# Kernel optimization log

Measured on AMD Instinct MI355X. Metric: run time of the kernel, lower is better.

## Reference

```python
import jax, jax.numpy as jnp
import numpy as np

NC = 80
CONF = 0.25
IOU_T = 0.45
MAX_DET = 100
ATTN_RES = 14
NUM_BASE = 5
TOPK = 1024          # candidate pre-filter (EfficientNMS-style)
SCALE = 0.25         # spatial_scale of ROIAlign


def setup_inputs() -> dict:
    key = jax.random.key(0)
    k1, k2, k3, k4 = jax.random.split(key, 4)
    B, A = 4, 25200
    test = jax.random.uniform(k1, (B, A, 5 + NC), dtype=jnp.float32)
    # scale boxes to image coords: cx,cy in [0,608), w,h in [0,120)
    box_scale = jnp.concatenate([jnp.array([608., 608., 120., 120.], jnp.float32),
                                 jnp.ones(1 + NC, jnp.float32)])
    test = test * box_scale
    attn = jax.random.normal(k2, (B, A, NUM_BASE * ATTN_RES * ATTN_RES), dtype=jnp.float32)
    bases = jax.random.normal(k3, (B, NUM_BASE - 1, 160, 160), dtype=jnp.float32)
    sem = jax.random.normal(k4, (B, 1, 160, 160), dtype=jnp.float32)
    return {"test": test, "attn": attn, "bases": bases, "sem": sem}


def _iou_matrix(b):
    # b: [K,4] xyxy
    area = jnp.clip(b[:, 2] - b[:, 0], 0) * jnp.clip(b[:, 3] - b[:, 1], 0)
    lt = jnp.maximum(b[:, None, :2], b[None, :, :2])
    rb = jnp.minimum(b[:, None, 2:], b[None, :, 2:])
    wh = jnp.clip(rb - lt, 0)
    inter = wh[..., 0] * wh[..., 1]
    return inter / (area[:, None] + area[None, :] - inter + 1e-9)


def _nms_single(boxes, scores):
    # boxes [A,4], scores [A,NC]. Class-aware greedy NMS over top-K candidates.
    flat = scores.reshape(-1)
    flat = jnp.where(flat > CONF, flat, -jnp.inf)
    top_s, top_i = jax.lax.top_k(flat, TOPK)
    anchor = top_i // NC
    cls = top_i % NC
    cb = boxes[anchor]                                   # [K,4]
    sup = (_iou_matrix(cb) > IOU_T) & (cls[:, None] == cls[None, :])

    def step(valid, _):
        s = jnp.where(valid, top_s, -jnp.inf)
        j = jnp.argmax(s)
        ok = jnp.isfinite(s[j])
        nv = (valid & ~sup[j]).at[j].set(False)
        return jnp.where(ok, nv, valid), (j, ok)

    _, (sel, selok) = jax.lax.scan(step, jnp.isfinite(top_s), None, length=MAX_DET)
    dboxes = jnp.where(selok[:, None], cb[sel], 0.)
    dscores = jnp.where(selok, top_s[sel], 0.)
    dcls = jnp.where(selok, cls[sel], 0).astype(jnp.int32)
    didx = jnp.where(selok, anchor[sel], 0).astype(jnp.int32)
    return selok.sum().astype(jnp.int32), dboxes, dscores, dcls, didx


def _roi_align(feat, rois, bidx, oh, ow, scale):
    # feat [B,C,H,W], rois [N,4] xyxy (input coords), half_pixel transform,
    # avg mode, 1 sample/bin (adaptive ratio = 1 here since bins < 1 px).
    N = rois.shape[0]
    B, C, H, W = feat.shape
    x1 = rois[:, 0] * scale - 0.5
    y1 = rois[:, 1] * scale - 0.5
    x2 = rois[:, 2] * scale - 0.5
    y2 = rois[:, 3] * scale - 0.5
    ys = y1[:, None] + (jnp.arange(oh, dtype=feat.dtype) + 0.5) * ((y2 - y1) / oh)[:, None]
    xs = x1[:, None] + (jnp.arange(ow, dtype=feat.dtype) + 0.5) * ((x2 - x1) / ow)[:, None]

    def axis(coord, dim):
        valid = (coord > -1.0) & (coord < dim)
        c = jnp.clip(coord, 0.0, dim - 1.0)
        lo = jnp.floor(c)
        hi = jnp.clip(lo + 1, 0, dim - 1)
        return lo.astype(jnp.int32), hi.astype(jnp.int32), c - lo, valid

    y0, y1i, wy, vy = axis(ys, H)
    x0, x1i, wx, vx = axis(xs, W)
    featn = feat[bidx]                                   # [N,C,H,W]
    n = jnp.arange(N)[:, None, None]

    def g(Y, X):  # -> [N,oh,ow,C]
        return featn[n, :, Y[:, :, None], X[:, None, :]]

    wy_ = wy[:, :, None, None]
    wx_ = wx[:, None, :, None]
    val = (g(y0, x0) * (1 - wy_) * (1 - wx_) + g(y0, x1i) * (1 - wy_) * wx_
           + g(y1i, x0) * wy_ * (1 - wx_) + g(y1i, x1i) * wy_ * wx_)
    val = jnp.where((vy[:, :, None] & vx[:, None, :])[..., None], val, 0.)
    return jnp.transpose(val, (0, 3, 1, 2))                # [N,C,oh,ow]


def _forward(test, attn, bases_in, sem):
    bases = jnp.concatenate([bases_in, sem], axis=1)       # [B,5,H,W]
    conv = jnp.array([[1, 0, 1, 0], [0, 1, 0, 1],
                      [-0.5, 0, 0.5, 0], [0, -0.5, 0, 0.5]], test.dtype)
    boxes = test[:, :, :4] @ conv                          # cxcywh -> xyxy
    scores = test[:, :, 5:5 + NC] * test[:, :, 4:5]
    _, dboxes, dscores, dcls, didx = jax.vmap(_nms_single)(boxes, scores)
    B, P, H, W = bases.shape
    bidx = jnp.repeat(jnp.arange(B), MAX_DET)              # [B*D]
    box_i = didx.reshape(-1)
    sel_boxes = boxes[bidx, box_i]                         # [N,4]
    sel_masks = attn[bidx, box_i]                          # [N,980]
    pooled = _roi_align(bases, sel_boxes, bidx, H, W, SCALE)  # [N,5,H,W]
    coeffs = sel_masks.reshape(-1, NUM_BASE, ATTN_RES, ATTN_RES)
    coeffs = jax.image.resize(coeffs, (coeffs.shape[0], NUM_BASE, H, W), 'linear')
    coeffs = jax.nn.softmax(coeffs, axis=1)
    masks = jax.nn.sigmoid((pooled * coeffs).sum(axis=1).reshape(B, MAX_DET, H * W))
    return jnp.concatenate([dboxes, dscores[..., None],
                            dcls.astype(test.dtype)[..., None], masks], axis=-1)


def reference(test, attn, bases, sem):
    return _forward(test, attn, bases, sem)
```

## Files before the change

kernel.cpp:

```cpp
#include <hip/hip_runtime.h>
#include <stdint.h>

#define B_   4
#define A_   25200
#define NC_  80
#define ROW_ 85
#define ATT_ 980
#define MAXDET_ 100
#define TOPK_ 1024
#define CAP_  4096
#define OUTSTRIDE_ 25606
#define HW_ 160
#define HWHW_ 25600
#define CONF_ 0.25f
#define IOUT_ 0.45f

#define WS_HIST 0
#define WS_CNT  4096
#define WS_TB   4160
#define WS_NTOP 4224
#define WS_CAND 8192
#define WS_TOPV 139264
#define WS_TOPA 155648
#define WS_TOPC 172032
#define WS_CB   188416
#define WS_SUP  253952
#define WS_DETA 778240

typedef unsigned long long u64;
typedef unsigned u32;

__global__ void k_clear(char* w) {
    int i = blockIdx.x * 256 + threadIdx.x;
    if (i < 1028) ((u32*)w)[i] = 0u;
}

__global__ void k_hist(const float* __restrict__ test, char* __restrict__ w) {
    int b = blockIdx.y;
    __shared__ u32 h[256];
    if (threadIdx.x < 256) h[threadIdx.x] = 0u;
    __syncthreads();
    const int total = A_ * NC_;
    for (int e = blockIdx.x * 256 + threadIdx.x; e < total; e += 128 * 256) {
        u32 a = (u32)e / 80u;
        u32 c = (u32)e - a * 80u;
        const float* row = test + ((size_t)b * A_ + a) * ROW_;
        float s = row[5 + c] * row[4];
        if (s > CONF_) {
            u32 key = __float_as_uint(s);
            int wb = (int)(key >> 17) - 7936;
            wb = wb < 0 ? 0 : (wb > 255 ? 255 : wb);
            atomicAdd(&h[wb], 1u);
        }
    }
    __syncthreads();
    u32* hist = (u32*)(w + WS_HIST);
    if (threadIdx.x < 256 && h[threadIdx.x]) atomicAdd(&hist[b * 256 + threadIdx.x], h[threadIdx.x]);
}

__global__ void k_thresh(char* w) {
    if (threadIdx.x < B_) {
        int b = threadIdx.x;
        const u32* h = (const u32*)(w + WS_HIST) + b * 256;
        u32 cum = 0; int wtb = 0;
        for (int i = 255; i >= 0; --i) {
            cum += h[i];
            if (cum >= TOPK_) { wtb = i; break; }
        }
        ((int*)(w + WS_TB))[b] = wtb;
    }
}

__global__ void k_collect(const float* __restrict__ test, char* __restrict__ w) {
    int b = blockIdx.y;
    int wtb = ((const int*)(w + WS_TB))[b];
    u32* cnt = (u32*)(w + WS_CNT);
    u64* cand = (u64*)(w + WS_CAND);
    const int total = A_ * NC_;
    for (int e = blockIdx.x * 256 + threadIdx.x; e < total; e += 128 * 256) {
        u32 a = (u32)e / 80u;
        u32 c = (u32)e - a * 80u;
        const float* row = test + ((size_t)b * A_ + a) * ROW_;
        float s = row[5 + c] * row[4];
        if (s > CONF_) {
            u32 key = __float_as_uint(s);
            int wb = (int)(key >> 17) - 7936;
            wb = wb < 0 ? 0 : (wb > 255 ? 255 : wb);
            if (wb >= wtb) {
                u32 pos = atomicAdd(&cnt[b], 1u);
                if (pos < CAP_)
                    cand[(size_t)b * CAP_ + pos] = ((u64)key << 32) | (u64)(0xFFFFFFFFu - (u32)e);
            }
        }
    }
}

__global__ __launch_bounds__(1024) void k_sort(const float* __restrict__ test, char* __restrict__ w) {
    int b = blockIdx.x;
    __shared__ u64 sm[CAP_];
    u32 cnt = ((const u32*)(w + WS_CNT))[b];
    int n = cnt < CAP_ ? (int)cnt : CAP_;
    const u64* cand = (const u64*)(w + WS_CAND) + (size_t)b * CAP_;
    for (int i = threadIdx.x; i < CAP_; i += 1024) sm[i] = (i < n) ? cand[i] : 0ull;
    __syncthreads();
    for (int k = 2; k <= CAP_; k <<= 1) {
        for (int j = k >> 1; j > 0; j >>= 1) {
            for (int t = threadIdx.x; t < CAP_; t += 1024) {
                int ixj = t ^ j;
                if (ixj > t) {
                    u64 a = sm[t], c = sm[ixj];
                    bool desc = ((t & k) == 0);
                    if (desc ? (a < c) : (a > c)) { sm[t] = c; sm[ixj] = a; }
                }
            }
            __syncthreads();
        }
    }
    int ntop = n < TOPK_ ? n : TOPK_;
    if (threadIdx.x == 0) ((int*)(w + WS_NTOP))[b] = ntop;
    if (threadIdx.x < TOPK_) {
        int i = threadIdx.x;
        float* topv = (float*)(w + WS_TOPV);
        int* topa = (int*)(w + WS_TOPA);
        int* topc = (int*)(w + WS_TOPC);
        float4* cb = (float4*)(w + WS_CB);
        if (i < ntop) {
            u64 v = sm[i];
            u32 key = (u32)(v >> 32);
            u32 idx = 0xFFFFFFFFu - (u32)(v & 0xFFFFFFFFull);
            u32 anchor = idx / 80u;
            u32 cls = idx - anchor * 80u;
            const float* tr = test + ((size_t)b * A_ + anchor) * ROW_;
            float cx = tr[0], cy = tr[1], ww = tr[2], hh = tr[3];
            float4 box;
            box.x = cx - 0.5f * ww; box.y = cy - 0.5f * hh;
            box.z = cx + 0.5f * ww; box.w = cy + 0.5f * hh;
            topv[b * TOPK_ + i] = __uint_as_float(key);
            topa[b * TOPK_ + i] = (int)anchor;
            topc[b * TOPK_ + i] = (int)cls;
            cb[b * TOPK_ + i] = box;
        } else {
            topv[b * TOPK_ + i] = 0.f;
            topa[b * TOPK_ + i] = 0;
            topc[b * TOPK_ + i] = 0;
            cb[b * TOPK_ + i] = make_float4(0.f, 0.f, 0.f, 0.f);
        }
    }
}

__device__ __forceinline__ bool sup_pair(float4 a, float4 b, int ca, int cbb) {
#pragma clang fp contract(off)
    if (ca != cbb) return false;
    float areaA = fmaxf(a.z - a.x, 0.f) * fmaxf(a.w - a.y, 0.f);
    float areaB = fmaxf(b.z - b.x, 0.f) * fmaxf(b.w - b.y, 0.f);
    float ltx = fmaxf(a.x, b.x), lty = fmaxf(a.y, b.y);
    float rbx = fminf(a.z, b.z), rby = fminf(a.w, b.w);
    float iw = fmaxf(rbx - ltx, 0.f), ih = fmaxf(rby - lty, 0.f);
    float inter = iw * ih;
    float iou = inter / (((areaA + areaB) - inter) + 1e-9f);
    return iou > IOUT_;
}

__global__ void k_sup(char* __restrict__ w) {
    int b = blockIdx.y;
    int t = blockIdx.x * 256 + threadIdx.x;
    int row = t >> 4, chunk = t & 15;
    const float4* cb = (const float4*)(w + WS_CB) + (size_t)b * TOPK_;
    const int* topc = (const int*)(w + WS_TOPC) + (size_t)b * TOPK_;
    float4 rb = cb[row];
    int rc = topc[row];
    u64 bits = 0ull;
    int base = chunk * 64;
    for (int cc = 0; cc < 64; ++cc) {
        if (sup_pair(rb, cb[base + cc], rc, topc[base + cc])) bits |= (1ull << cc);
    }
    ((u64*)(w + WS_SUP))[((size_t)b * TOPK_ + row) * 16 + chunk] = bits;
}

__global__ void k_nms(char* __restrict__ w, float* __restrict__ out) {
    int b = blockIdx.x;
    int lane = threadIdx.x;
    int ntop = ((const int*)(w + WS_NTOP))[b];
    const u64* sup = (const u64*)(w + WS_SUP);
    __shared__ int selA[MAXDET_];
    __shared__ int okA[MAXDET_];
    u32 valid = 0u;
    for (int t = 0; t < 16; ++t)
        if (lane * 16 + t < ntop) valid |= (1u << t);
    for (int k = 0; k < MAXDET_; ++k) {
        u64 bal = __ballot(valid != 0u);
        if (bal == 0ull) {
            if (lane == 0) { selA[k] = 0; okA[k] = 0; }
            continue;
        }
        int L = __ffsll(bal) - 1;
        u32 vL = (u32)__shfl((int)valid, L);
        int j = L * 16 + (__ffs(vL & 0xFFFFu) - 1);
        u64 chunk = sup[((size_t)b * TOPK_ + j) * 16 + (lane >> 2)];
        u32 s16 = (u32)(chunk >> ((lane & 3) * 16)) & 0xFFFFu;
        valid &= ~s16;
        if (lane == L) valid &= ~(1u << (j & 15));
        if (lane == 0) { selA[k] = j; okA[k] = 1; }
    }
    __syncthreads();
    const float* topv = (const float*)(w + WS_TOPV) + (size_t)b * TOPK_;
    const int* topa = (const int*)(w + WS_TOPA) + (size_t)b * TOPK_;
    const int* topc = (const int*)(w + WS_TOPC) + (size_t)b * TOPK_;
    const float4* cb = (const float4*)(w + WS_CB) + (size_t)b * TOPK_;
    int* deta = (int*)(w + WS_DETA);
    for (int k = lane; k < MAXDET_; k += 64) {
        int ok = okA[k], s = selA[k];
        float b0 = 0, b1 = 0, b2 = 0, b3 = 0, sc = 0; int cls_ = 0, anc = 0;
        if (ok) {
            float4 bb = cb[s];
            b0 = bb.x; b1 = bb.y; b2 = bb.z; b3 = bb.w;
            sc = topv[s]; cls_ = topc[s]; anc = topa[s];
        }
        size_t o = ((size_t)(b * MAXDET_ + k)) * OUTSTRIDE_;
        out[o + 0] = b0; out[o + 1] = b1; out[o + 2] = b2; out[o + 3] = b3;
        out[o + 4] = sc; out[o + 5] = (float)cls_;
        deta[b * MAXDET_ + k] = anc;
    }
}

__global__ void k_mask(const float* __restrict__ test, const float* __restrict__ attn,
                       const float* __restrict__ bases, const float* __restrict__ sem,
                       const char* __restrict__ w, float* __restrict__ out) {
    int roi = blockIdx.x;
    int b = roi / MAXDET_;
    int anchor = ((const int*)(w + WS_DETA))[roi];
    const float* t = test + ((size_t)b * A_ + anchor) * ROW_;
    float cx = t[0], cy = t[1], ww = t[2], hh = t[3];
    float bx1 = cx - 0.5f * ww, by1 = cy - 0.5f * hh;
    float bx2 = cx + 0.5f * ww, by2 = cy + 0.5f * hh;
    float rx1 = bx1 * 0.25f - 0.5f, ry1 = by1 * 0.25f - 0.5f;
    float rx2 = bx2 * 0.25f - 0.5f, ry2 = by2 * 0.25f - 0.5f;
    float xstep = (rx2 - rx1) / 160.f, ystep = (ry2 - ry1) / 160.f;

    __shared__ float att[5 * 196];
    __shared__ float sxw[HW_], syw[HW_], rzw[HW_];
    __shared__ int sxlo[HW_], sxhi[HW_], sylo[HW_], syhi[HW_];
    __shared__ int sxv[HW_], syv[HW_], rzlo[HW_];

    const float* arow = attn + ((size_t)b * A_ + anchor) * ATT_;
    for (int i = threadIdx.x; i < ATT_; i += 256) att[i] = arow[i];
    if (threadIdx.x < HW_) {
        int i = threadIdx.x;
        float coord = rx1 + (i + 0.5f) * xstep;
        sxv[i] = (coord > -1.0f) && (coord < 160.0f);
        float c = fminf(fmaxf(coord, 0.f), 159.f);
        float lo = floorf(c);
        sxlo[i] = (int)lo; sxhi[i] = min((int)lo + 1, 159); sxw[i] = c - lo;
        coord = ry1 + (i + 0.5f) * ystep;
        syv[i] = (coord > -1.0f) && (coord < 160.0f);
        c = fminf(fmaxf(coord, 0.f), 159.f);
        lo = floorf(c);
        sylo[i] = (int)lo; syhi[i] = min((int)lo + 1, 159); syw[i] = c - lo;
        float f = (i + 0.5f) * (14.f / 160.f) - 0.5f;
        float rc = fminf(fmaxf(f, 0.f), 13.f);
        float rlo = floorf(rc);
        rzlo[i] = (int)rlo; rzw[i] = rc - rlo;
    }
    __syncthreads();

    const float* bp[5];
    bp[0] = bases + ((size_t)b * 4 + 0) * HWHW_;
    bp[1] = bases + ((size_t)b * 4 + 1) * HWHW_;
    bp[2] = bases + ((size_t)b * 4 + 2) * HWHW_;
    bp[3] = bases + ((size_t)b * 4 + 3) * HWHW_;
    bp[4] = sem + (size_t)b * HWHW_;

    size_t obase = (size_t)roi * OUTSTRIDE_ + 6;
    int pstart = blockIdx.y * (HWHW_ / 8);
    int pend = pstart + (HWHW_ / 8);
    for (int p = pstart + (int)threadIdx.x; p < pend; p += 256) {
        int y = p / HW_, x = p - y * HW_;
        int ylo = sylo[y], yhi = syhi[y]; float wy = syw[y];
        int xlo = sxlo[x], xhi = sxhi[x]; float wx = sxw[x];
        bool v = sxv[x] && syv[y];
        float w00 = (1.f - wy) * (1.f - wx), w01 = (1.f - wy) * wx;
        float w10 = wy * (1.f - wx), w11 = wy * wx;
        int i00 = ylo * HW_ + xlo, i01 = ylo * HW_ + xhi;
        int i10 = yhi * HW_ + xlo, i11 = yhi * HW_ + xhi;
        float pooled[5];
#pragma unroll
        for (int c5 = 0; c5 < 5; ++c5) {
            float g = bp[c5][i00] * w00 + bp[c5][i01] * w01 + bp[c5][i10] * w10 + bp[c5][i11] * w11;
            pooled[c5] = v ? g : 0.f;
        }
        int cylo = rzlo[y]; float cwy = rzw[y]; int cyhi = min(cylo + 1, 13);
        int cxlo = rzlo[x]; float cwx = rzw[x]; int cxhi = min(cxlo + 1, 13);
        float c00 = (1.f - cwy) * (1.f - cwx), c01 = (1.f - cwy) * cwx;
        float c10 = cwy * (1.f - cwx), c11 = cwy * cwx;
        int j00 = cylo * 14 + cxlo, j01 = cylo * 14 + cxhi;
        int j10 = cyhi * 14 + cxlo, j11 = cyhi * 14 + cxhi;
        float cf[5]; float m = -1e30f;
#pragma unroll
        for (int c5 = 0; c5 < 5; ++c5) {
            const float* ap = att + c5 * 196;
            float g = ap[j00] * c00 + ap[j01] * c01 + ap[j10] * c10 + ap[j11] * c11;
            cf[c5] = g; m = fmaxf(m, g);
        }
        float se = 0.f, dot = 0.f;
#pragma unroll
        for (int c5 = 0; c5 < 5; ++c5) {
            float e = __expf(cf[c5] - m);
            se += e; dot += pooled[c5] * e;
        }
        dot /= se;
        out[obase + p] = 1.f / (1.f + __expf(-dot));
    }
}

extern "C" void kernel_launch(void* const* d_in, const int* in_sizes, int n_in,
                              void* d_out, int out_size, void* d_ws, size_t ws_size,
                              hipStream_t stream) {
    const float* test = (const float*)d_in[0];
    const float* attn = (const float*)d_in[1];
    const float* bases = (const float*)d_in[2];
    const float* sem = (const float*)d_in[3];
    float* out = (float*)d_out;
    char* w = (char*)d_ws;

    k_clear<<<5, 256, 0, stream>>>(w);
    k_hist<<<dim3(128, B_), 256, 0, stream>>>(test, w);
    k_thresh<<<1, 64, 0, stream>>>(w);
    k_collect<<<dim3(128, B_), 256, 0, stream>>>(test, w);
    k_sort<<<B_, 1024, 0, stream>>>(test, w);
    k_sup<<<dim3(64, B_), 256, 0, stream>>>(w);
    k_nms<<<B_, 64, 0, stream>>>(w, out);
    k_mask<<<dim3(B_ * MAXDET_, 8), 256, 0, stream>>>(test, attn, bases, sem, w, out);
}
```

Measured before the change: 709.4 us.

## Fuse sort, suppression and NMS into one block kernel; fold threshold into collect

Removes the threshold kernel by computing a suffix-sum over the histogram inside each collect block. Merges sort, suppression-matrix build and greedy NMS into one 1024-thread kernel per batch that keeps candidates in shared memory and evaluates IoU on the fly for only the chosen row at each step. The bitonic sort now runs on the next power of two at or above the candidate count instead of a fixed 4096. This cuts three launches and the global suppression matrix, but adds two block-wide barriers per NMS step and a serial scan by thread 0.

Measured after the change: 694.9 us. 1.02x faster.

```diff
diff --git a/kernel.cpp b/kernel.cpp
--- a/kernel.cpp
+++ b/kernel.cpp
@@ -17,15 +17,8 @@
 
 #define WS_HIST 0
 #define WS_CNT  4096
-#define WS_TB   4160
-#define WS_NTOP 4224
 #define WS_CAND 8192
-#define WS_TOPV 139264
-#define WS_TOPA 155648
-#define WS_TOPC 172032
-#define WS_CB   188416
-#define WS_SUP  253952
-#define WS_DETA 778240
+#define WS_DETA 139264
 
 typedef unsigned long long u64;
 typedef unsigned u32;
@@ -58,22 +51,32 @@
     if (threadIdx.x < 256 && h[threadIdx.x]) atomicAdd(&hist[b * 256 + threadIdx.x], h[threadIdx.x]);
 }
 
-__global__ void k_thresh(char* w) {
-    if (threadIdx.x < B_) {
-        int b = threadIdx.x;
-        const u32* h = (const u32*)(w + WS_HIST) + b * 256;
-        u32 cum = 0; int wtb = 0;
-        for (int i = 255; i >= 0; --i) {
-            cum += h[i];
-            if (cum >= TOPK_) { wtb = i; break; }
-        }
-        ((int*)(w + WS_TB))[b] = wtb;
-    }
-}
-
 __global__ void k_collect(const float* __restrict__ test, char* __restrict__ w) {
     int b = blockIdx.y;
-    int wtb = ((const int*)(w + WS_TB))[b];
+    __shared__ u32 s[256];
+    __shared__ int swtb;
+    const u32* hist = (const u32*)(w + WS_HIST) + (size_t)b * 256;
+    if (threadIdx.x < 256) s[threadIdx.x] = hist[threadIdx.x];
+    if (threadIdx.x == 0) swtb = 0;
+    __syncthreads();
+    for (int off = 1; off < 256; off <<= 1) {
+        u32 v = 0;
+        if (threadIdx.x < 256) {
+            v = s[threadIdx.x];
+            if (threadIdx.x + off < 256) v += s[threadIdx.x + off];
+        }
+        __syncthreads();
+        if (threadIdx.x < 256) s[threadIdx.x] = v;
+        __syncthreads();
+    }
+    if (threadIdx.x < 256) {
+        u32 Si = s[threadIdx.x];
+        u32 Sn = (threadIdx.x == 255) ? 0u : s[threadIdx.x + 1];
+        if (Si >= TOPK_ && Sn < TOPK_) swtb = threadIdx.x;
+    }
+    __syncthreads();
+    int wtb = swtb;
+
     u32* cnt = (u32*)(w + WS_CNT);
     u64* cand = (u64*)(w + WS_CAND);
     const int total = A_ * NC_;
@@ -81,9 +84,9 @@
         u32 a = (u32)e / 80u;
         u32 c = (u32)e - a * 80u;
         const float* row = test + ((size_t)b * A_ + a) * ROW_;
-        float s = row[5 + c] * row[4];
-        if (s > CONF_) {
-            u32 key = __float_as_uint(s);
+        float sc = row[5 + c] * row[4];
+        if (sc > CONF_) {
+            u32 key = __float_as_uint(sc);
             int wb = (int)(key >> 17) - 7936;
             wb = wb < 0 ? 0 : (wb > 255 ? 255 : wb);
             if (wb >= wtb) {
@@ -95,17 +98,44 @@
     }
 }
 
-__global__ __launch_bounds__(1024) void k_sort(const float* __restrict__ test, char* __restrict__ w) {
+__device__ __forceinline__ bool sup_pair(float4 a, float4 b, int ca, int cbb) {
+#pragma clang fp contract(off)
+    if (ca != cbb) return false;
+    float areaA = fmaxf(a.z - a.x, 0.f) * fmaxf(a.w - a.y, 0.f);
+    float areaB = fmaxf(b.z - b.x, 0.f) * fmaxf(b.w - b.y, 0.f);
+    float ltx = fmaxf(a.x, b.x), lty = fmaxf(a.y, b.y);
+    float rbx = fminf(a.z, b.z), rby = fminf(a.w, b.w);
+    float iw = fmaxf(rbx - ltx, 0.f), ih = fmaxf(rby - lty, 0.f);
+    float inter = iw * ih;
+    float iou = inter / (((areaA + areaB) - inter) + 1e-9f);
+    return iou > IOUT_;
+}
+
+__global__ __launch_bounds__(1024) void k_sortnms(const float* __restrict__ test,
+                                                  char* __restrict__ w,
+                                                  float* __restrict__ out) {
     int b = blockIdx.x;
+    int tid = threadIdx.x;
     __shared__ u64 sm[CAP_];
+    __shared__ float4 cbs[TOPK_];
+    __shared__ float tvs[TOPK_];
+    __shared__ int tcs[TOPK_];
+    __shared__ int tas[TOPK_];
+    __shared__ u64 wmask[16];
+    __shared__ int selA[MAXDET_];
+    __shared__ u32 okA[MAXDET_];
+    __shared__ int sj;
+
     u32 cnt = ((const u32*)(w + WS_CNT))[b];
     int n = cnt < CAP_ ? (int)cnt : CAP_;
+    int n2 = 1024;
+    while (n2 < n) n2 <<= 1;
     const u64* cand = (const u64*)(w + WS_CAND) + (size_t)b * CAP_;
-    for (int i = threadIdx.x; i < CAP_; i += 1024) sm[i] = (i < n) ? cand[i] : 0ull;
-    __syncthreads();
-    for (int k = 2; k <= CAP_; k <<= 1) {
+    for (int i = tid; i < n2; i += 1024) sm[i] = (i < n) ? cand[i] : 0ull;
+    __syncthreads();
+    for (int k = 2; k <= n2; k <<= 1) {
         for (int j = k >> 1; j > 0; j >>= 1) {
-            for (int t = threadIdx.x; t < CAP_; t += 1024) {
+            for (int t = tid; t < n2; t += 1024) {
                 int ixj = t ^ j;
                 if (ixj > t) {
                     u64 a = sm[t], c = sm[ixj];
@@ -117,13 +147,8 @@
         }
     }
     int ntop = n < TOPK_ ? n : TOPK_;
-    if (threadIdx.x == 0) ((int*)(w + WS_NTOP))[b] = ntop;
-    if (threadIdx.x < TOPK_) {
-        int i = threadIdx.x;
-        float* topv = (float*)(w + WS_TOPV);
-        int* topa = (int*)(w + WS_TOPA);
-        int* topc = (int*)(w + WS_TOPC);
-        float4* cb = (float4*)(w + WS_CB);
+    {
+        int i = tid;
         if (i < ntop) {
             u64 v = sm[i];
             u32 key = (u32)(v >> 32);
@@ -135,86 +160,48 @@
             float4 box;
             box.x = cx - 0.5f * ww; box.y = cy - 0.5f * hh;
             box.z = cx + 0.5f * ww; box.w = cy + 0.5f * hh;
-            topv[b * TOPK_ + i] = __uint_as_float(key);
-            topa[b * TOPK_ + i] = (int)anchor;
-            topc[b * TOPK_ + i] = (int)cls;
-            cb[b * TOPK_ + i] = box;
+            tvs[i] = __uint_as_float(key);
+            tas[i] = (int)anchor; tcs[i] = (int)cls; cbs[i] = box;
         } else {
-            topv[b * TOPK_ + i] = 0.f;
-            topa[b * TOPK_ + i] = 0;
-            topc[b * TOPK_ + i] = 0;
-            cb[b * TOPK_ + i] = make_float4(0.f, 0.f, 0.f, 0.f);
-        }
-    }
-}
-
-__device__ __forceinline__ bool sup_pair(float4 a, float4 b, int ca, int cbb) {
-#pragma clang fp contract(off)
-    if (ca != cbb) return false;
-    float areaA = fmaxf(a.z - a.x, 0.f) * fmaxf(a.w - a.y, 0.f);
-    float areaB = fmaxf(b.z - b.x, 0.f) * fmaxf(b.w - b.y, 0.f);
-    float ltx = fmaxf(a.x, b.x), lty = fmaxf(a.y, b.y);
-    float rbx = fminf(a.z, b.z), rby = fminf(a.w, b.w);
-    float iw = fmaxf(rbx - ltx, 0.f), ih = fmaxf(rby - lty, 0.f);
-    float inter = iw * ih;
-    float iou = inter / (((areaA + areaB) - inter) + 1e-9f);
-    return iou > IOUT_;
-}
-
-__global__ void k_sup(char* __restrict__ w) {
-    int b = blockIdx.y;
-    int t = blockIdx.x * 256 + threadIdx.x;
-    int row = t >> 4, chunk = t & 15;
-    const float4* cb = (const float4*)(w + WS_CB) + (size_t)b * TOPK_;
-    const int* topc = (const int*)(w + WS_TOPC) + (size_t)b * TOPK_;
-    float4 rb = cb[row];
-    int rc = topc[row];
-    u64 bits = 0ull;
-    int base = chunk * 64;
-    for (int cc = 0; cc < 64; ++cc) {
-        if (sup_pair(rb, cb[base + cc], rc, topc[base + cc])) bits |= (1ull << cc);
-    }
-    ((u64*)(w + WS_SUP))[((size_t)b * TOPK_ + row) * 16 + chunk] = bits;
-}
-
-__global__ void k_nms(char* __restrict__ w, float* __restrict__ out) {
-    int b = blockIdx.x;
-    int lane = threadIdx.x;
-    int ntop = ((const int*)(w + WS_NTOP))[b];
-    const u64* sup = (const u64*)(w + WS_SUP);
-    __shared__ int selA[MAXDET_];
-    __shared__ int okA[MAXDET_];
-    u32 valid = 0u;
-    for (int t = 0; t < 16; ++t)
-        if (lane * 16 + t < ntop) valid |= (1u << t);
+            tvs[i] = 0.f; tas[i] = 0; tcs[i] = 0;
+            cbs[i] = make_float4(0.f, 0.f, 0.f, 0.f);
+        }
+    }
+    __syncthreads();
+
+    bool valid = (tid < ntop);
+    float4 myb = cbs[tid];
+    int myc = tcs[tid];
     for (int k = 0; k < MAXDET_; ++k) {
-        u64 bal = __ballot(valid != 0u);
-        if (bal == 0ull) {
-            if (lane == 0) { selA[k] = 0; okA[k] = 0; }
-            continue;
-        }
-        int L = __ffsll(bal) - 1;
-        u32 vL = (u32)__shfl((int)valid, L);
-        int j = L * 16 + (__ffs(vL & 0xFFFFu) - 1);
-        u64 chunk = sup[((size_t)b * TOPK_ + j) * 16 + (lane >> 2)];
-        u32 s16 = (u32)(chunk >> ((lane & 3) * 16)) & 0xFFFFu;
-        valid &= ~s16;
-        if (lane == L) valid &= ~(1u << (j & 15));
-        if (lane == 0) { selA[k] = j; okA[k] = 1; }
-    }
-    __syncthreads();
-    const float* topv = (const float*)(w + WS_TOPV) + (size_t)b * TOPK_;
-    const int* topa = (const int*)(w + WS_TOPA) + (size_t)b * TOPK_;
-    const int* topc = (const int*)(w + WS_TOPC) + (size_t)b * TOPK_;
-    const float4* cb = (const float4*)(w + WS_CB) + (size_t)b * TOPK_;
+        u64 bal = __ballot(valid);
+        if ((tid & 63) == 0) wmask[tid >> 6] = bal;
+        __syncthreads();
+        if (tid == 0) {
+            int j = -1;
+            for (int wv = 15; wv >= 0; --wv) {
+                u64 m = wmask[wv];
+                if (m) j = (wv << 6) + (__ffsll(m) - 1);
+            }
+            sj = j;
+            selA[k] = j < 0 ? 0 : j;
+            okA[k] = j < 0 ? 0u : 1u;
+        }
+        __syncthreads();
+        int j = sj;
+        if (j >= 0 && valid) {
+            if (tid == j || sup_pair(cbs[j], myb, tcs[j], myc)) valid = false;
+        }
+    }
+    __syncthreads();
+
     int* deta = (int*)(w + WS_DETA);
-    for (int k = lane; k < MAXDET_; k += 64) {
-        int ok = okA[k], s = selA[k];
+    for (int k = tid; k < MAXDET_; k += 1024) {
+        int ok = (int)okA[k], s = selA[k];
         float b0 = 0, b1 = 0, b2 = 0, b3 = 0, sc = 0; int cls_ = 0, anc = 0;
         if (ok) {
-            float4 bb = cb[s];
+            float4 bb = cbs[s];
             b0 = bb.x; b1 = bb.y; b2 = bb.z; b3 = bb.w;
-            sc = topv[s]; cls_ = topc[s]; anc = topa[s];
+            sc = tvs[s]; cls_ = tcs[s]; anc = tas[s];
         }
         size_t o = ((size_t)(b * MAXDET_ + k)) * OUTSTRIDE_;
         out[o + 0] = b0; out[o + 1] = b1; out[o + 2] = b2; out[o + 3] = b3;
@@ -324,10 +311,7 @@
 
     k_clear<<<5, 256, 0, stream>>>(w);
     k_hist<<<dim3(128, B_), 256, 0, stream>>>(test, w);
-    k_thresh<<<1, 64, 0, stream>>>(w);
     k_collect<<<dim3(128, B_), 256, 0, stream>>>(test, w);
-    k_sort<<<B_, 1024, 0, stream>>>(test, w);
-    k_sup<<<dim3(64, B_), 256, 0, stream>>>(w);
-    k_nms<<<B_, 64, 0, stream>>>(w, out);
+    k_sortnms<<<B_, 1024, 0, stream>>>(test, w, out);
     k_mask<<<dim3(B_ * MAXDET_, 8), 256, 0, stream>>>(test, attn, bases, sem, w, out);
 }
```
